# Kernel tuning notes

Hardware: AMD Instinct MI355X
Metric: run time of the kernel (lower is better)

The kernel has to match this reference:

```python
import jax, jax.numpy as jnp
import numpy as np

HEADS = 4
DIM_HEAD = 32
GROUPS = 32  # min(256//4, 32)
EPS = 1e-5


def setup_inputs() -> dict:
    key = jax.random.key(0)
    ks = jax.random.split(key, 6)
    B, C, H, W = 16, 256, 64, 64
    hidden = HEADS * DIM_HEAD  # 128
    return {
        "x": jax.random.normal(ks[0], (B, C, H, W), dtype=jnp.float32),
        "gn_w": jax.random.uniform(ks[1], (C,), dtype=jnp.float32),
        "gn_b": jax.random.normal(ks[2], (C,), dtype=jnp.float32) * 0.05,
        "qkv_w": jax.random.normal(ks[3], (3 * hidden, C), dtype=jnp.float32) * 0.05,
        "qkv_b": jax.random.normal(ks[4], (3 * hidden,), dtype=jnp.float32) * 0.05,
        "out_w": jax.random.normal(ks[5], (C, hidden), dtype=jnp.float32) * 0.05,
        "out_b": jnp.zeros((C,), dtype=jnp.float32),
    }


def _forward_single(x, gn_w, gn_b, qkv_w, qkv_b, out_w, out_b):
    # x: (c, h, w)
    c, h, w = x.shape
    # GroupNorm over (channels-in-group, h, w)
    xg = x.reshape(GROUPS, c // GROUPS, h, w)
    mean = xg.mean(axis=(1, 2, 3), keepdims=True)
    var = xg.var(axis=(1, 2, 3), keepdims=True)
    xn = ((xg - mean) * jax.lax.rsqrt(var + EPS)).reshape(c, h, w)
    xn = xn * gn_w[:, None, None] + gn_b[:, None, None]
    # 1x1 conv QKV projection
    qkv = jnp.einsum('oc,chw->ohw', qkv_w, xn) + qkv_b[:, None, None]
    qkv = qkv.reshape(3, HEADS, DIM_HEAD, h * w)
    q, k, v = qkv[0], qkv[1], qkv[2]
    k = jax.nn.softmax(k, axis=-1)  # softmax over spatial
    context = jnp.einsum('hdn,hen->hde', k, v)   # (heads, d, d)
    out = jnp.einsum('hde,hdn->hen', context, q)  # (heads, d, n)
    out = out.reshape(HEADS * DIM_HEAD, h, w)
    # 1x1 conv output projection
    return jnp.einsum('oc,chw->ohw', out_w, out) + out_b[:, None, None]


def reference(x, gn_w, gn_b, qkv_w, qkv_b, out_w, out_b):
    f = lambda xi: _forward_single(xi, gn_w, gn_b, qkv_w, qkv_b, out_w, out_b)
    return jax.vmap(f)(x)
```

## Files before the change

kernel.cpp:

```cpp
#include <hip/hip_runtime.h>
#include <stdint.h>

typedef unsigned short u16;
typedef __attribute__((ext_vector_type(8))) short bf16x8;
typedef __attribute__((ext_vector_type(4))) float f32x4;

#define B_   16
#define C_   256
#define HW_  4096
#define QR_  384
#define HID_ 128

__device__ __forceinline__ float b2f(u16 u) {
  union { uint32_t i; float f; } v; v.i = ((uint32_t)u) << 16; return v.f;
}
__device__ __forceinline__ u16 f2b(float f) {
  union { float f; uint32_t i; } v; v.f = f;
  uint32_t r = (v.i + 0x7FFFu + ((v.i >> 16) & 1u)) >> 16;
  return (u16)r;
}

__global__ __launch_bounds__(256) void convw_kernel(
    const float* __restrict__ src, u16* __restrict__ dst, int n4)
{
  int i = blockIdx.x * 256 + threadIdx.x;
  if (i >= n4) return;
  float4 f = ((const float4*)src)[i];
  ushort4 o;
  o.x = f2b(f.x); o.y = f2b(f.y); o.z = f2b(f.z); o.w = f2b(f.w);
  ((ushort4*)dst)[i] = o;
}

__global__ __launch_bounds__(256) void gn_stats_kernel(
    const float* __restrict__ x, const float* __restrict__ gnw,
    const float* __restrict__ gnb, float* __restrict__ scale,
    float* __restrict__ shiftv)
{
  int b = blockIdx.x >> 5, g = blockIdx.x & 31;
  const float* p = x + ((size_t)b * C_ + g * 8) * HW_;
  int t = threadIdx.x;
  float s = 0.f, sq = 0.f;
#pragma unroll
  for (int i = 0; i < 16; ++i) {
    float4 u0 = *(const float4*)(p + t * 8 + i * 2048);
    float4 u1 = *(const float4*)(p + t * 8 + i * 2048 + 4);
    s  += u0.x + u0.y + u0.z + u0.w + u1.x + u1.y + u1.z + u1.w;
    sq += u0.x*u0.x + u0.y*u0.y + u0.z*u0.z + u0.w*u0.w
        + u1.x*u1.x + u1.y*u1.y + u1.z*u1.z + u1.w*u1.w;
  }
#pragma unroll
  for (int off = 32; off > 0; off >>= 1) {
    s  += __shfl_down(s, off);
    sq += __shfl_down(sq, off);
  }
  __shared__ float ps[4], pq[4], mr[2];
  int lane = t & 63, w = t >> 6;
  if (lane == 0) { ps[w] = s; pq[w] = sq; }
  __syncthreads();
  if (t == 0) {
    float S = ps[0] + ps[1] + ps[2] + ps[3];
    float Q = pq[0] + pq[1] + pq[2] + pq[3];
    float mean = S * (1.f / 32768.f);
    float var  = Q * (1.f / 32768.f) - mean * mean;
    mr[0] = mean; mr[1] = rsqrtf(var + 1e-5f);
  }
  __syncthreads();
  if (t < 8) {
    int c = g * 8 + t;
    float sc = gnw[c] * mr[1];
    scale[b * C_ + c]  = sc;
    shiftv[b * C_ + c] = gnb[c] - mr[0] * sc;
  }
}

__global__ __launch_bounds__(256) void gn_transpose_kernel(
    const float* __restrict__ x, u16* __restrict__ dst,
    const float* __restrict__ scale, const float* __restrict__ shiftv)
{
  int nt = blockIdx.x, ct = blockIdx.y, b = blockIdx.z;
  const float* S = x + (size_t)b * C_ * HW_;
  u16* D = dst + (size_t)b * HW_ * C_;
  __shared__ __align__(16) u16 tile[64][136];
  int t = threadIdx.x;
  int n0 = nt * 128, c0 = ct * 64;
  int r = t >> 2, seg = (t & 3) * 32;
  float sc = scale[(size_t)b * C_ + c0 + r];
  float sh = shiftv[(size_t)b * C_ + c0 + r];
#pragma unroll
  for (int i = 0; i < 4; ++i) {
    const float* rp = S + (size_t)(c0 + r) * HW_ + n0 + seg + i * 8;
    float4 u0 = *(const float4*)(rp);
    float4 u1 = *(const float4*)(rp + 4);
    float f[8] = {u0.x, u0.y, u0.z, u0.w, u1.x, u1.y, u1.z, u1.w};
    uint4 o;
    uint32_t* op = (uint32_t*)&o;
#pragma unroll
    for (int j = 0; j < 4; ++j) {
      op[j] = (uint32_t)f2b(f[2 * j] * sc + sh)
            | ((uint32_t)f2b(f[2 * j + 1] * sc + sh) << 16);
    }
    *(uint4*)&tile[r][seg + i * 8] = o;
  }
  __syncthreads();
#pragma unroll
  for (int i = 0; i < 4; ++i) {
    int m = t * 4 + i;
    int n_l = m >> 3, cg = (m & 7) * 8;
    union { u16 v[8]; uint4 q; } pk;
#pragma unroll
    for (int e = 0; e < 8; ++e) pk.v[e] = tile[cg + e][n_l];
    *(uint4*)(D + (size_t)(n0 + n_l) * C_ + c0 + cg) = pk.q;
  }
}

__global__ __launch_bounds__(256) void qt_transpose_kernel(
    const u16* __restrict__ qkv, u16* __restrict__ dst)
{
  int nt = blockIdx.x, ct = blockIdx.y, b = blockIdx.z;
  const u16* S = qkv + (size_t)b * QR_ * HW_;
  u16* D = dst + (size_t)b * HW_ * HID_;
  __shared__ __align__(16) u16 tile[64][136];
  int t = threadIdx.x;
  int n0 = nt * 128, c0 = ct * 64;
  int r = t >> 2, seg = (t & 3) * 32;
#pragma unroll
  for (int i = 0; i < 4; ++i) {
    uint4 u = *(const uint4*)(S + (size_t)(c0 + r) * HW_ + n0 + seg + i * 8);
    *(uint4*)&tile[r][seg + i * 8] = u;
  }
  __syncthreads();
#pragma unroll
  for (int i = 0; i < 4; ++i) {
    int m = t * 4 + i;
    int n_l = m >> 3, cg = (m & 7) * 8;
    union { u16 v[8]; uint4 q; } pk;
#pragma unroll
    for (int e = 0; e < 8; ++e) pk.v[e] = tile[cg + e][n_l];
    *(uint4*)(D + (size_t)(n0 + n_l) * HID_ + c0 + cg) = pk.q;
  }
}

template<bool OUTF32>
__global__ __launch_bounds__(256) void gemm_bt_kernel(
    const u16* __restrict__ A, long long aBS,
    const u16* __restrict__ Bt, long long bBS,
    const float* __restrict__ bias,
    void* __restrict__ Cout, long long cBS, int K)
{
  int nt = blockIdx.x, mt = blockIdx.y, b = blockIdx.z;
  const u16* Ab = A + (size_t)b * aBS + (size_t)mt * 128 * K;
  const u16* Bb = Bt + (size_t)b * bBS + (size_t)nt * 128 * K;
  __shared__ __align__(16) u16 lA[128 * 32];
  __shared__ __align__(16) u16 lB[128 * 32];
  int t = threadIdx.x;
  int lane = t & 63, w = t >> 6;
  int quad = lane >> 4, l16 = lane & 15;
  int wm = (w >> 1) * 64, wn = (w & 1) * 64;
  f32x4 acc[4][4];
#pragma unroll
  for (int i = 0; i < 4; ++i)
#pragma unroll
    for (int j = 0; j < 4; ++j)
#pragma unroll
      for (int r = 0; r < 4; ++r) acc[i][j][r] = 0.f;

  for (int k0 = 0; k0 < K; k0 += 32) {
    __syncthreads();
#pragma unroll
    for (int q = 0; q < 2; ++q) {
      int ch = q * 256 + t;
      int row = ch >> 2, off = (ch & 3) * 8;
      __builtin_amdgcn_global_load_lds(
          (const __attribute__((address_space(1))) void*)(Ab + (size_t)row * K + k0 + off),
          (__attribute__((address_space(3))) void*)(lA + ch * 8), 16, 0, 0);
      __builtin_amdgcn_global_load_lds(
          (const __attribute__((address_space(1))) void*)(Bb + (size_t)row * K + k0 + off),
          (__attribute__((address_space(3))) void*)(lB + ch * 8), 16, 0, 0);
    }
    __syncthreads();
    const bf16x8* A8 = (const bf16x8*)lA;
    const bf16x8* B8 = (const bf16x8*)lB;
    bf16x8 af[4], bfr[4];
#pragma unroll
    for (int i = 0; i < 4; ++i) af[i]  = A8[(wm + i * 16 + l16) * 4 + quad];
#pragma unroll
    for (int j = 0; j < 4; ++j) bfr[j] = B8[(wn + j * 16 + l16) * 4 + quad];
#pragma unroll
    for (int i = 0; i < 4; ++i)
#pragma unroll
      for (int j = 0; j < 4; ++j)
        acc[i][j] = __builtin_amdgcn_mfma_f32_16x16x32_bf16(af[i], bfr[j],
                                                            acc[i][j], 0, 0, 0);
  }
#pragma unroll
  for (int i = 0; i < 4; ++i) {
#pragma unroll
    for (int rg = 0; rg < 4; ++rg) {
      int o = mt * 128 + wm + i * 16 + quad * 4 + rg;
      float bsv = bias[o];
      size_t rowbase = (size_t)b * cBS + (size_t)o * HW_;
#pragma unroll
      for (int j = 0; j < 4; ++j) {
        int n = nt * 128 + wn + j * 16 + l16;
        float val = acc[i][j][rg] + bsv;
        if (OUTF32) ((float*)Cout)[rowbase + n] = val;
        else        ((u16*)Cout)[rowbase + n] = f2b(val);
      }
    }
  }
}

__global__ __launch_bounds__(256) void softmax_kernel(u16* __restrict__ qkv)
{
  int row = blockIdx.x;
  int b = row >> 7, r = row & 127;
  u16* p = qkv + ((size_t)b * QR_ + 128 + r) * HW_;
  int t = threadIdx.x;
  float x[16];
  uint4 u0 = *(const uint4*)(p + t * 16);
  uint4 u1 = *(const uint4*)(p + t * 16 + 8);
  {
    uint32_t wds[8] = {u0.x, u0.y, u0.z, u0.w, u1.x, u1.y, u1.z, u1.w};
#pragma unroll
    for (int j = 0; j < 8; ++j) {
      x[2 * j]     = b2f((u16)(wds[j] & 0xffffu));
      x[2 * j + 1] = b2f((u16)(wds[j] >> 16));
    }
  }
  float m = x[0];
#pragma unroll
  for (int i = 1; i < 16; ++i) m = fmaxf(m, x[i]);
#pragma unroll
  for (int off = 32; off > 0; off >>= 1) m = fmaxf(m, __shfl_down(m, off));
  __shared__ float buf[4];
  int lane = t & 63, w = t >> 6;
  if (lane == 0) buf[w] = m;
  __syncthreads();
  m = fmaxf(fmaxf(buf[0], buf[1]), fmaxf(buf[2], buf[3]));
  __syncthreads();
  float s = 0.f;
#pragma unroll
  for (int i = 0; i < 16; ++i) { x[i] = __expf(x[i] - m); s += x[i]; }
#pragma unroll
  for (int off = 32; off > 0; off >>= 1) s += __shfl_down(s, off);
  if (lane == 0) buf[w] = s;
  __syncthreads();
  s = buf[0] + buf[1] + buf[2] + buf[3];
  float inv = 1.f / s;
  uint4 o0, o1;
  uint32_t* op0 = (uint32_t*)&o0;
  uint32_t* op1 = (uint32_t*)&o1;
#pragma unroll
  for (int j = 0; j < 4; ++j) {
    op0[j] = (uint32_t)f2b(x[2 * j] * inv) | ((uint32_t)f2b(x[2 * j + 1] * inv) << 16);
    op1[j] = (uint32_t)f2b(x[8 + 2 * j] * inv) | ((uint32_t)f2b(x[8 + 2 * j + 1] * inv) << 16);
  }
  *(uint4*)(p + t * 16) = o0;
  *(uint4*)(p + t * 16 + 8) = o1;
}

__global__ __launch_bounds__(256) void ctxwf_kernel(
    const u16* __restrict__ qkv, const float* __restrict__ outw,
    u16* __restrict__ wf)
{
  int b = blockIdx.x >> 2, h = blockIdx.x & 3;
  const u16* kb = qkv + ((size_t)b * QR_ + 128 + h * 32) * HW_;
  const u16* vb = qkv + ((size_t)b * QR_ + 256 + h * 32) * HW_;
  int t = threadIdx.x;
  int w = t >> 6, lane = t & 63;
  int quad = lane >> 4, l16 = lane & 15;
  __shared__ float part[4][1024];
  __shared__ float cs[1024];
  f32x4 acc[2][2];
#pragma unroll
  for (int i = 0; i < 2; ++i)
#pragma unroll
    for (int j = 0; j < 2; ++j)
#pragma unroll
      for (int r = 0; r < 4; ++r) acc[i][j][r] = 0.f;
  int kbase = w * 1024;
  for (int it = 0; it < 32; ++it) {
    int k0 = kbase + it * 32;
    bf16x8 a0 = *(const bf16x8*)(kb + (size_t)l16 * HW_ + k0 + quad * 8);
    bf16x8 a1 = *(const bf16x8*)(kb + (size_t)(16 + l16) * HW_ + k0 + quad * 8);
    bf16x8 b0 = *(const bf16x8*)(vb + (size_t)l16 * HW_ + k0 + quad * 8);
    bf16x8 b1 = *(const bf16x8*)(vb + (size_t)(16 + l16) * HW_ + k0 + quad * 8);
    acc[0][0] = __builtin_amdgcn_mfma_f32_16x16x32_bf16(a0, b0, acc[0][0], 0, 0, 0);
    acc[0][1] = __builtin_amdgcn_mfma_f32_16x16x32_bf16(a0, b1, acc[0][1], 0, 0, 0);
    acc[1][0] = __builtin_amdgcn_mfma_f32_16x16x32_bf16(a1, b0, acc[1][0], 0, 0, 0);
    acc[1][1] = __builtin_amdgcn_mfma_f32_16x16x32_bf16(a1, b1, acc[1][1], 0, 0, 0);
  }
#pragma unroll
  for (int i = 0; i < 2; ++i)
#pragma unroll
    for (int j = 0; j < 2; ++j)
#pragma unroll
      for (int r = 0; r < 4; ++r) {
        int d = i * 16 + quad * 4 + r;
        int e = j * 16 + l16;
        part[w][d * 32 + e] = acc[i][j][r];
      }
  __syncthreads();
#pragma unroll
  for (int i = 0; i < 4; ++i) {
    int idx = t + i * 256;
    cs[idx] = part[0][idx] + part[1][idx] + part[2][idx] + part[3][idx];
  }
  __syncthreads();
  float wv[32];
  const float* wr = outw + (size_t)t * HID_ + h * 32;
#pragma unroll
  for (int e = 0; e < 32; ++e) wv[e] = wr[e];
  for (int d = 0; d < 32; ++d) {
    float a = 0.f;
#pragma unroll
    for (int e = 0; e < 32; ++e) a += wv[e] * cs[d * 32 + e];
    wf[((size_t)b * C_ + t) * HID_ + h * 32 + d] = f2b(a);
  }
}

extern "C" void kernel_launch(void* const* d_in, const int* in_sizes, int n_in,
                              void* d_out, int out_size, void* d_ws, size_t ws_size,
                              hipStream_t stream)
{
  const float* x    = (const float*)d_in[0];
  const float* gnw  = (const float*)d_in[1];
  const float* gnb  = (const float*)d_in[2];
  const float* qkvw = (const float*)d_in[3];
  const float* qkvb = (const float*)d_in[4];
  const float* outw = (const float*)d_in[5];
  const float* outb = (const float*)d_in[6];

  char* p = (char*)d_ws;
  float* scale  = (float*)p;            p += (size_t)B_ * C_ * 4;
  float* shiftv = (float*)p;            p += (size_t)B_ * C_ * 4;
  u16* cqkvw = (u16*)p;                 p += (size_t)QR_ * C_ * 2;
  u16* xn_t  = (u16*)p;                 p += (size_t)B_ * HW_ * C_ * 2;
  u16* qkv   = (u16*)p;                 p += (size_t)B_ * QR_ * HW_ * 2;
  u16* q_t   = (u16*)p;                 p += (size_t)B_ * HW_ * HID_ * 2;
  u16* wf    = (u16*)p;

  convw_kernel<<<(QR_ * C_ / 4 + 255) / 256, 256, 0, stream>>>(qkvw, cqkvw, QR_ * C_ / 4);
  gn_stats_kernel<<<512, 256, 0, stream>>>(x, gnw, gnb, scale, shiftv);
  gn_transpose_kernel<<<dim3(32, 4, 16), 256, 0, stream>>>(x, xn_t, scale, shiftv);
  gemm_bt_kernel<false><<<dim3(32, 3, 16), 256, 0, stream>>>(
      cqkvw, 0, xn_t, (long long)HW_ * C_, qkvb, qkv, (long long)QR_ * HW_, C_);
  softmax_kernel<<<2048, 256, 0, stream>>>(qkv);
  qt_transpose_kernel<<<dim3(32, 2, 16), 256, 0, stream>>>(qkv, q_t);
  ctxwf_kernel<<<64, 256, 0, stream>>>(qkv, outw, wf);
  gemm_bt_kernel<true><<<dim3(32, 2, 16), 256, 0, stream>>>(
      wf, (long long)C_ * HID_, q_t, (long long)HW_ * HID_, outb, d_out,
      (long long)C_ * HW_, HID_);
}
```

Before: 225.7 us.

## Fuse Q transpose into QKV GEMM epilogue and softmax into context kernel

The QKV GEMM now writes the Q block transposed through shared memory straight into q_t, so the separate transpose kernel goes away. The K softmax is folded into the context kernel, which runs 1024 threads per block, computes row max and sum with an online reduction, and applies exp on the fly before the MFMA. The GEMMs now use a K-step of 64 with two MFMA sub-steps per tile. This removes two launches and a round trip of the K rows through memory. In exchange, K is read twice inside the context kernel, and that kernel still has only 64 blocks.

```diff
diff --git a/kernel.cpp b/kernel.cpp
--- a/kernel.cpp
+++ b/kernel.cpp
@@ -113,45 +113,18 @@
   }
 }
 
-__global__ __launch_bounds__(256) void qt_transpose_kernel(
-    const u16* __restrict__ qkv, u16* __restrict__ dst)
-{
-  int nt = blockIdx.x, ct = blockIdx.y, b = blockIdx.z;
-  const u16* S = qkv + (size_t)b * QR_ * HW_;
-  u16* D = dst + (size_t)b * HW_ * HID_;
-  __shared__ __align__(16) u16 tile[64][136];
-  int t = threadIdx.x;
-  int n0 = nt * 128, c0 = ct * 64;
-  int r = t >> 2, seg = (t & 3) * 32;
-#pragma unroll
-  for (int i = 0; i < 4; ++i) {
-    uint4 u = *(const uint4*)(S + (size_t)(c0 + r) * HW_ + n0 + seg + i * 8);
-    *(uint4*)&tile[r][seg + i * 8] = u;
-  }
-  __syncthreads();
-#pragma unroll
-  for (int i = 0; i < 4; ++i) {
-    int m = t * 4 + i;
-    int n_l = m >> 3, cg = (m & 7) * 8;
-    union { u16 v[8]; uint4 q; } pk;
-#pragma unroll
-    for (int e = 0; e < 8; ++e) pk.v[e] = tile[cg + e][n_l];
-    *(uint4*)(D + (size_t)(n0 + n_l) * HID_ + c0 + cg) = pk.q;
-  }
-}
-
-template<bool OUTF32>
-__global__ __launch_bounds__(256) void gemm_bt_kernel(
-    const u16* __restrict__ A, long long aBS,
-    const u16* __restrict__ Bt, long long bBS,
-    const float* __restrict__ bias,
-    void* __restrict__ Cout, long long cBS, int K)
-{
+__global__ __launch_bounds__(256) void qkv_gemm_kernel(
+    const u16* __restrict__ A, const u16* __restrict__ Bt,
+    const float* __restrict__ bias, u16* __restrict__ qkv,
+    u16* __restrict__ q_t)
+{
+  const int K = C_;
   int nt = blockIdx.x, mt = blockIdx.y, b = blockIdx.z;
-  const u16* Ab = A + (size_t)b * aBS + (size_t)mt * 128 * K;
-  const u16* Bb = Bt + (size_t)b * bBS + (size_t)nt * 128 * K;
-  __shared__ __align__(16) u16 lA[128 * 32];
-  __shared__ __align__(16) u16 lB[128 * 32];
+  const u16* Ab = A + (size_t)mt * 128 * K;
+  const u16* Bb = Bt + (size_t)b * HW_ * C_ + (size_t)nt * 128 * K;
+  __shared__ __align__(16) u16 smem[128 * 136];
+  u16* lA = smem;
+  u16* lB = smem + 8192;
   int t = threadIdx.x;
   int lane = t & 63, w = t >> 6;
   int quad = lane >> 4, l16 = lane & 15;
@@ -164,12 +137,12 @@
 #pragma unroll
       for (int r = 0; r < 4; ++r) acc[i][j][r] = 0.f;
 
-  for (int k0 = 0; k0 < K; k0 += 32) {
-    __syncthreads();
-#pragma unroll
-    for (int q = 0; q < 2; ++q) {
+  for (int k0 = 0; k0 < K; k0 += 64) {
+    __syncthreads();
+#pragma unroll
+    for (int q = 0; q < 4; ++q) {
       int ch = q * 256 + t;
-      int row = ch >> 2, off = (ch & 3) * 8;
+      int row = ch >> 3, off = (ch & 7) * 8;
       __builtin_amdgcn_global_load_lds(
           (const __attribute__((address_space(1))) void*)(Ab + (size_t)row * K + k0 + off),
           (__attribute__((address_space(3))) void*)(lA + ch * 8), 16, 0, 0);
@@ -180,86 +153,63 @@
     __syncthreads();
     const bf16x8* A8 = (const bf16x8*)lA;
     const bf16x8* B8 = (const bf16x8*)lB;
-    bf16x8 af[4], bfr[4];
-#pragma unroll
-    for (int i = 0; i < 4; ++i) af[i]  = A8[(wm + i * 16 + l16) * 4 + quad];
-#pragma unroll
-    for (int j = 0; j < 4; ++j) bfr[j] = B8[(wn + j * 16 + l16) * 4 + quad];
-#pragma unroll
-    for (int i = 0; i < 4; ++i)
-#pragma unroll
-      for (int j = 0; j < 4; ++j)
-        acc[i][j] = __builtin_amdgcn_mfma_f32_16x16x32_bf16(af[i], bfr[j],
-                                                            acc[i][j], 0, 0, 0);
-  }
-#pragma unroll
-  for (int i = 0; i < 4; ++i) {
-#pragma unroll
-    for (int rg = 0; rg < 4; ++rg) {
-      int o = mt * 128 + wm + i * 16 + quad * 4 + rg;
-      float bsv = bias[o];
-      size_t rowbase = (size_t)b * cBS + (size_t)o * HW_;
+#pragma unroll
+    for (int kk = 0; kk < 2; ++kk) {
+      bf16x8 af[4], bfr[4];
+#pragma unroll
+      for (int i = 0; i < 4; ++i) af[i]  = A8[(wm + i * 16 + l16) * 8 + kk * 4 + quad];
+#pragma unroll
+      for (int j = 0; j < 4; ++j) bfr[j] = B8[(wn + j * 16 + l16) * 8 + kk * 4 + quad];
+#pragma unroll
+      for (int i = 0; i < 4; ++i)
+#pragma unroll
+        for (int j = 0; j < 4; ++j)
+          acc[i][j] = __builtin_amdgcn_mfma_f32_16x16x32_bf16(af[i], bfr[j],
+                                                              acc[i][j], 0, 0, 0);
+    }
+  }
+
+  if (mt == 0) {
+    __syncthreads();
+#pragma unroll
+    for (int i = 0; i < 4; ++i) {
+      int o0 = wm + i * 16 + quad * 4;
+      float b0 = bias[o0], b1 = bias[o0 + 1], b2 = bias[o0 + 2], b3 = bias[o0 + 3];
 #pragma unroll
       for (int j = 0; j < 4; ++j) {
-        int n = nt * 128 + wn + j * 16 + l16;
-        float val = acc[i][j][rg] + bsv;
-        if (OUTF32) ((float*)Cout)[rowbase + n] = val;
-        else        ((u16*)Cout)[rowbase + n] = f2b(val);
+        int n_l = wn + j * 16 + l16;
+        uint2 pk;
+        pk.x = (uint32_t)f2b(acc[i][j][0] + b0) | ((uint32_t)f2b(acc[i][j][1] + b1) << 16);
+        pk.y = (uint32_t)f2b(acc[i][j][2] + b2) | ((uint32_t)f2b(acc[i][j][3] + b3) << 16);
+        *(uint2*)&smem[n_l * 136 + o0] = pk;
       }
     }
-  }
-}
-
-__global__ __launch_bounds__(256) void softmax_kernel(u16* __restrict__ qkv)
-{
-  int row = blockIdx.x;
-  int b = row >> 7, r = row & 127;
-  u16* p = qkv + ((size_t)b * QR_ + 128 + r) * HW_;
-  int t = threadIdx.x;
-  float x[16];
-  uint4 u0 = *(const uint4*)(p + t * 16);
-  uint4 u1 = *(const uint4*)(p + t * 16 + 8);
-  {
-    uint32_t wds[8] = {u0.x, u0.y, u0.z, u0.w, u1.x, u1.y, u1.z, u1.w};
-#pragma unroll
-    for (int j = 0; j < 8; ++j) {
-      x[2 * j]     = b2f((u16)(wds[j] & 0xffffu));
-      x[2 * j + 1] = b2f((u16)(wds[j] >> 16));
-    }
-  }
-  float m = x[0];
-#pragma unroll
-  for (int i = 1; i < 16; ++i) m = fmaxf(m, x[i]);
-#pragma unroll
-  for (int off = 32; off > 0; off >>= 1) m = fmaxf(m, __shfl_down(m, off));
-  __shared__ float buf[4];
-  int lane = t & 63, w = t >> 6;
-  if (lane == 0) buf[w] = m;
-  __syncthreads();
-  m = fmaxf(fmaxf(buf[0], buf[1]), fmaxf(buf[2], buf[3]));
-  __syncthreads();
-  float s = 0.f;
-#pragma unroll
-  for (int i = 0; i < 16; ++i) { x[i] = __expf(x[i] - m); s += x[i]; }
-#pragma unroll
-  for (int off = 32; off > 0; off >>= 1) s += __shfl_down(s, off);
-  if (lane == 0) buf[w] = s;
-  __syncthreads();
-  s = buf[0] + buf[1] + buf[2] + buf[3];
-  float inv = 1.f / s;
-  uint4 o0, o1;
-  uint32_t* op0 = (uint32_t*)&o0;
-  uint32_t* op1 = (uint32_t*)&o1;
-#pragma unroll
-  for (int j = 0; j < 4; ++j) {
-    op0[j] = (uint32_t)f2b(x[2 * j] * inv) | ((uint32_t)f2b(x[2 * j + 1] * inv) << 16);
-    op1[j] = (uint32_t)f2b(x[8 + 2 * j] * inv) | ((uint32_t)f2b(x[8 + 2 * j + 1] * inv) << 16);
-  }
-  *(uint4*)(p + t * 16) = o0;
-  *(uint4*)(p + t * 16 + 8) = o1;
-}
-
-__global__ __launch_bounds__(256) void ctxwf_kernel(
+    __syncthreads();
+    int n_l = t >> 1, half = t & 1;
+    u16* dst = q_t + (size_t)b * HW_ * HID_ + (size_t)(nt * 128 + n_l) * HID_ + half * 64;
+    const u16* srcp = smem + n_l * 136 + half * 64;
+#pragma unroll
+    for (int i = 0; i < 8; ++i)
+      *(uint4*)(dst + i * 8) = *(const uint4*)(srcp + i * 8);
+  } else {
+#pragma unroll
+    for (int i = 0; i < 4; ++i) {
+#pragma unroll
+      for (int rg = 0; rg < 4; ++rg) {
+        int o = mt * 128 + wm + i * 16 + quad * 4 + rg;
+        float bsv = bias[o];
+        size_t rowbase = (size_t)b * QR_ * HW_ + (size_t)o * HW_;
+#pragma unroll
+        for (int j = 0; j < 4; ++j) {
+          int n = nt * 128 + wn + j * 16 + l16;
+          qkv[rowbase + n] = f2b(acc[i][j][rg] + bsv);
+        }
+      }
+    }
+  }
+}
+
+__global__ __launch_bounds__(1024) void ctxwf_kernel(
     const u16* __restrict__ qkv, const float* __restrict__ outw,
     u16* __restrict__ wf)
 {
@@ -268,9 +218,45 @@
   const u16* vb = qkv + ((size_t)b * QR_ + 256 + h * 32) * HW_;
   int t = threadIdx.x;
   int w = t >> 6, lane = t & 63;
+  __shared__ float part[16][1024];
+  __shared__ float cs[1024];
+  __shared__ float mrow[32], srow[32];
+
+  {
+    int row = t >> 5, sub = t & 31;
+    const u16* rp = kb + (size_t)row * HW_;
+    float m = -3.0e38f, s = 0.f;
+#pragma unroll
+    for (int it = 0; it < 16; ++it) {
+      bf16x8 v8 = *(const bf16x8*)(rp + sub * 8 + it * 256);
+      const u16* e8 = (const u16*)&v8;
+      float f[8];
+#pragma unroll
+      for (int e = 0; e < 8; ++e) f[e] = b2f(e8[e]);
+      float lm = fmaxf(fmaxf(fmaxf(f[0], f[1]), fmaxf(f[2], f[3])),
+                       fmaxf(fmaxf(f[4], f[5]), fmaxf(f[6], f[7])));
+      float mn = fmaxf(m, lm);
+      float ls = 0.f;
+#pragma unroll
+      for (int e = 0; e < 8; ++e) ls += __expf(f[e] - mn);
+      s = s * __expf(m - mn) + ls;
+      m = mn;
+    }
+#pragma unroll
+    for (int off = 16; off > 0; off >>= 1) {
+      float om = __shfl_down(m, off);
+      float os = __shfl_down(s, off);
+      float mn = fmaxf(m, om);
+      s = s * __expf(m - mn) + os * __expf(om - mn);
+      m = mn;
+    }
+    if ((lane & 31) == 0) { mrow[row] = m; srow[row] = s; }
+  }
+  __syncthreads();
+
   int quad = lane >> 4, l16 = lane & 15;
-  __shared__ float part[4][1024];
-  __shared__ float cs[1024];
+  float m0 = mrow[l16],      is0 = 1.f / srow[l16];
+  float m1 = mrow[16 + l16], is1 = 1.f / srow[16 + l16];
   f32x4 acc[2][2];
 #pragma unroll
   for (int i = 0; i < 2; ++i)
@@ -278,17 +264,25 @@
     for (int j = 0; j < 2; ++j)
 #pragma unroll
       for (int r = 0; r < 4; ++r) acc[i][j][r] = 0.f;
-  int kbase = w * 1024;
-  for (int it = 0; it < 32; ++it) {
-    int k0 = kbase + it * 32;
-    bf16x8 a0 = *(const bf16x8*)(kb + (size_t)l16 * HW_ + k0 + quad * 8);
-    bf16x8 a1 = *(const bf16x8*)(kb + (size_t)(16 + l16) * HW_ + k0 + quad * 8);
-    bf16x8 b0 = *(const bf16x8*)(vb + (size_t)l16 * HW_ + k0 + quad * 8);
-    bf16x8 b1 = *(const bf16x8*)(vb + (size_t)(16 + l16) * HW_ + k0 + quad * 8);
-    acc[0][0] = __builtin_amdgcn_mfma_f32_16x16x32_bf16(a0, b0, acc[0][0], 0, 0, 0);
-    acc[0][1] = __builtin_amdgcn_mfma_f32_16x16x32_bf16(a0, b1, acc[0][1], 0, 0, 0);
-    acc[1][0] = __builtin_amdgcn_mfma_f32_16x16x32_bf16(a1, b0, acc[1][0], 0, 0, 0);
-    acc[1][1] = __builtin_amdgcn_mfma_f32_16x16x32_bf16(a1, b1, acc[1][1], 0, 0, 0);
+  int kbase = w * 256;
+  for (int it = 0; it < 8; ++it) {
+    int n0 = kbase + it * 32 + quad * 8;
+    bf16x8 k0 = *(const bf16x8*)(kb + (size_t)l16 * HW_ + n0);
+    bf16x8 k1 = *(const bf16x8*)(kb + (size_t)(16 + l16) * HW_ + n0);
+    bf16x8 v0 = *(const bf16x8*)(vb + (size_t)l16 * HW_ + n0);
+    bf16x8 v1 = *(const bf16x8*)(vb + (size_t)(16 + l16) * HW_ + n0);
+    bf16x8 a0, a1;
+    const u16* k0p = (const u16*)&k0; u16* a0p = (u16*)&a0;
+    const u16* k1p = (const u16*)&k1; u16* a1p = (u16*)&a1;
+#pragma unroll
+    for (int e = 0; e < 8; ++e) {
+      a0p[e] = f2b(__expf(b2f(k0p[e]) - m0) * is0);
+      a1p[e] = f2b(__expf(b2f(k1p[e]) - m1) * is1);
+    }
+    acc[0][0] = __builtin_amdgcn_mfma_f32_16x16x32_bf16(a0, v0, acc[0][0], 0, 0, 0);
+    acc[0][1] = __builtin_amdgcn_mfma_f32_16x16x32_bf16(a0, v1, acc[0][1], 0, 0, 0);
+    acc[1][0] = __builtin_amdgcn_mfma_f32_16x16x32_bf16(a1, v0, acc[1][0], 0, 0, 0);
+    acc[1][1] = __builtin_amdgcn_mfma_f32_16x16x32_bf16(a1, v1, acc[1][1], 0, 0, 0);
   }
 #pragma unroll
   for (int i = 0; i < 2; ++i)
@@ -301,21 +295,97 @@
         part[w][d * 32 + e] = acc[i][j][r];
       }
   __syncthreads();
+  {
+    float a = 0.f;
+#pragma unroll
+    for (int ww = 0; ww < 16; ++ww) a += part[ww][t];
+    cs[t] = a;
+  }
+  __syncthreads();
+
+  int o = t & 255, dg = t >> 8;
+  const float* wr = outw + (size_t)o * HID_ + h * 32;
+  float wv[32];
+#pragma unroll
+  for (int e = 0; e < 32; ++e) wv[e] = wr[e];
+  union { u16 v[8]; uint4 q; } pk;
+#pragma unroll
+  for (int dd = 0; dd < 8; ++dd) {
+    int d = dg * 8 + dd;
+    float a = 0.f;
+#pragma unroll
+    for (int e = 0; e < 32; ++e) a += wv[e] * cs[d * 32 + e];
+    pk.v[dd] = f2b(a);
+  }
+  *(uint4*)(wf + ((size_t)b * C_ + o) * HID_ + h * 32 + dg * 8) = pk.q;
+}
+
+__global__ __launch_bounds__(256) void out_gemm_kernel(
+    const u16* __restrict__ A, const u16* __restrict__ Bt,
+    const float* __restrict__ bias, float* __restrict__ Cout)
+{
+  const int K = HID_;
+  int nt = blockIdx.x, mt = blockIdx.y, b = blockIdx.z;
+  const u16* Ab = A + (size_t)b * C_ * HID_ + (size_t)mt * 128 * K;
+  const u16* Bb = Bt + (size_t)b * HW_ * HID_ + (size_t)nt * 128 * K;
+  __shared__ __align__(16) u16 lA[128 * 64];
+  __shared__ __align__(16) u16 lB[128 * 64];
+  int t = threadIdx.x;
+  int lane = t & 63, w = t >> 6;
+  int quad = lane >> 4, l16 = lane & 15;
+  int wm = (w >> 1) * 64, wn = (w & 1) * 64;
+  f32x4 acc[4][4];
+#pragma unroll
+  for (int i = 0; i < 4; ++i)
+#pragma unroll
+    for (int j = 0; j < 4; ++j)
+#pragma unroll
+      for (int r = 0; r < 4; ++r) acc[i][j][r] = 0.f;
+
+  for (int k0 = 0; k0 < K; k0 += 64) {
+    __syncthreads();
+#pragma unroll
+    for (int q = 0; q < 4; ++q) {
+      int ch = q * 256 + t;
+      int row = ch >> 3, off = (ch & 7) * 8;
+      __builtin_amdgcn_global_load_lds(
+          (const __attribute__((address_space(1))) void*)(Ab + (size_t)row * K + k0 + off),
+          (__attribute__((address_space(3))) void*)(lA + ch * 8), 16, 0, 0);
+      __builtin_amdgcn_global_load_lds(
+          (const __attribute__((address_space(1))) void*)(Bb + (size_t)row * K + k0 + off),
+          (__attribute__((address_space(3))) void*)(lB + ch * 8), 16, 0, 0);
+    }
+    __syncthreads();
+    const bf16x8* A8 = (const bf16x8*)lA;
+    const bf16x8* B8 = (const bf16x8*)lB;
+#pragma unroll
+    for (int kk = 0; kk < 2; ++kk) {
+      bf16x8 af[4], bfr[4];
+#pragma unroll
+      for (int i = 0; i < 4; ++i) af[i]  = A8[(wm + i * 16 + l16) * 8 + kk * 4 + quad];
+#pragma unroll
+      for (int j = 0; j < 4; ++j) bfr[j] = B8[(wn + j * 16 + l16) * 8 + kk * 4 + quad];
+#pragma unroll
+      for (int i = 0; i < 4; ++i)
+#pragma unroll
+        for (int j = 0; j < 4; ++j)
+          acc[i][j] = __builtin_amdgcn_mfma_f32_16x16x32_bf16(af[i], bfr[j],
+                                                              acc[i][j], 0, 0, 0);
+    }
+  }
 #pragma unroll
   for (int i = 0; i < 4; ++i) {
-    int idx = t + i * 256;
-    cs[idx] = part[0][idx] + part[1][idx] + part[2][idx] + part[3][idx];
-  }
-  __syncthreads();
-  float wv[32];
-  const float* wr = outw + (size_t)t * HID_ + h * 32;
-#pragma unroll
-  for (int e = 0; e < 32; ++e) wv[e] = wr[e];
-  for (int d = 0; d < 32; ++d) {
-    float a = 0.f;
-#pragma unroll
-    for (int e = 0; e < 32; ++e) a += wv[e] * cs[d * 32 + e];
-    wf[((size_t)b * C_ + t) * HID_ + h * 32 + d] = f2b(a);
+#pragma unroll
+    for (int rg = 0; rg < 4; ++rg) {
+      int o = mt * 128 + wm + i * 16 + quad * 4 + rg;
+      float bsv = bias[o];
+      size_t rowbase = (size_t)b * C_ * HW_ + (size_t)o * HW_;
+#pragma unroll
+      for (int j = 0; j < 4; ++j) {
+        int n = nt * 128 + wn + j * 16 + l16;
+        Cout[rowbase + n] = acc[i][j][rg] + bsv;
+      }
+    }
   }
 }
 
@@ -343,12 +413,7 @@
   convw_kernel<<<(QR_ * C_ / 4 + 255) / 256, 256, 0, stream>>>(qkvw, cqkvw, QR_ * C_ / 4);
   gn_stats_kernel<<<512, 256, 0, stream>>>(x, gnw, gnb, scale, shiftv);
   gn_transpose_kernel<<<dim3(32, 4, 16), 256, 0, stream>>>(x, xn_t, scale, shiftv);
-  gemm_bt_kernel<false><<<dim3(32, 3, 16), 256, 0, stream>>>(
-      cqkvw, 0, xn_t, (long long)HW_ * C_, qkvb, qkv, (long long)QR_ * HW_, C_);
-  softmax_kernel<<<2048, 256, 0, stream>>>(qkv);
-  qt_transpose_kernel<<<dim3(32, 2, 16), 256, 0, stream>>>(qkv, q_t);
-  ctxwf_kernel<<<64, 256, 0, stream>>>(qkv, outw, wf);
-  gemm_bt_kernel<true><<<dim3(32, 2, 16), 256, 0, stream>>>(
-      wf, (long long)C_ * HID_, q_t, (long long)HW_ * HID_, outb, d_out,
-      (long long)C_ * HW_, HID_);
-}
+  qkv_gemm_kernel<<<dim3(32, 3, 16), 256, 0, stream>>>(cqkvw, xn_t, qkvb, qkv, q_t);
+  ctxwf_kernel<<<64, 1024, 0, stream>>>(qkv, outw, wf);
+  out_gemm_kernel<<<dim3(32, 2, 16), 256, 0, stream>>>(wf, q_t, outb, (float*)d_out);
+}
```

New measurement: 217.9 us. 3.5% less time.
